# Kernel tuning notes

Hardware: AMD Instinct MI355X
Metric: run time of the kernel (lower is better)

## Reference

```python
import jax, jax.numpy as jnp
import numpy as np

B, S, E, H = 1, 2048, 512, 8
D = E // H
N = B * S
WIN_HALF = 32  # attention_window 64 -> +/-32
ALPHA = 0.1
LN_EPS = 1e-12
NEG_INF = -1e9


def _build_window_edges():
    # windowed graph: dst i attends to src j with |i-j| <= WIN_HALF, within each batch block
    i = np.arange(S)
    offs = np.arange(-WIN_HALF, WIN_HALF + 1)
    src = i[:, None] + offs[None, :]
    dst = np.broadcast_to(i[:, None], src.shape)
    valid = (src >= 0) & (src < S)
    src, dst = src[valid], dst[valid]
    srcs, dsts = [], []
    for b in range(B):
        srcs.append(src + b * S)
        dsts.append(dst + b * S)
    return (np.concatenate(srcs).astype(np.int32),
            np.concatenate(dsts).astype(np.int32))


def setup_inputs() -> dict:
    key = jax.random.key(0)
    ks = jax.random.split(key, 12)
    sc = 1.0 / np.sqrt(E)
    src_np, dst_np = _build_window_edges()
    return {
        "hidden_states": jax.random.normal(ks[0], (B, S, E), dtype=jnp.float32),
        "attention_mask": jnp.zeros((B, S), dtype=jnp.float32),
        "edge_src": jnp.asarray(src_np),
        "edge_dst": jnp.asarray(dst_np),
        "Wq": jax.random.normal(ks[1], (E, E), dtype=jnp.float32) * sc,
        "bq": jnp.zeros((E,), dtype=jnp.float32),
        "Wk": jax.random.normal(ks[2], (E, E), dtype=jnp.float32) * sc,
        "bk": jnp.zeros((E,), dtype=jnp.float32),
        "Wv": jax.random.normal(ks[3], (E, E), dtype=jnp.float32) * sc,
        "bv": jnp.zeros((E,), dtype=jnp.float32),
        "Wo": jax.random.normal(ks[4], (E, E), dtype=jnp.float32) * sc,
        "bo": jnp.zeros((E,), dtype=jnp.float32),
        "ln_g": jnp.ones((E,), dtype=jnp.float32),
        "ln_b": jnp.zeros((E,), dtype=jnp.float32),
    }


def reference(hidden_states, attention_mask, edge_src, edge_dst,
              Wq, bq, Wk, bk, Wv, bv, Wo, bo, ln_g, ln_b):
    x = hidden_states  # (B,S,E); node ordering n = b*S + s (matches torch reshape)
    q = ((x @ Wq + bq) / jnp.sqrt(jnp.asarray(D, x.dtype))).reshape(N, H, D)
    k = (x @ Wk + bk).reshape(N, H, D)
    v = (x @ Wv + bv).reshape(N, H, D)

    mask = (attention_mask >= 0).reshape(N)  # bool per node

    # u_dot_v('k','q','score'): per-edge, per-head dot product
    score = jnp.einsum('ehd,ehd->eh', k[edge_src], q[edge_dst])  # (Eg,H)
    score = jnp.where(mask[edge_src][:, None], score, NEG_INF)

    # edge_softmax over incoming edges of each destination node
    smax = jax.ops.segment_max(score, edge_dst, num_segments=N)
    p = jnp.exp(score - smax[edge_dst])
    denom = jax.ops.segment_sum(p, edge_dst, num_segments=N)
    p = p / denom[edge_dst]  # (Eg,H)

    # 5 diffusion steps: h <- A h, blended with residual v (dropout off in eval)
    h = v
    for _ in range(5):
        m = h[edge_src] * p[:, :, None]                      # u_mul_e
        h = jax.ops.segment_sum(m, edge_dst, num_segments=N)  # sum('m','h')
        h = (1.0 - ALPHA) * h + ALPHA * v

    attn = h.reshape(B, S, E)

    # DiffuserSelfOutput: dense -> residual add -> LayerNorm
    y = attn @ Wo + bo + hidden_states
    mu = y.mean(-1, keepdims=True)
    var = ((y - mu) ** 2).mean(-1, keepdims=True)
    out = (y - mu) * jax.lax.rsqrt(var + LN_EPS) * ln_g + ln_b
    return out
```

## Files before the change

### kernel.cpp

```cpp
#include <hip/hip_runtime.h>
#include <math.h>

#define S_LEN 2048
#define E_DIM 512
#define NE (S_LEN * E_DIM)
#define H_NUM 8
#define WH 32
#define NOFF 65
#define PROW (H_NUM * NOFF)
#define PN (S_LEN * PROW)

typedef float f32x4 __attribute__((ext_vector_type(4)));
typedef short short8 __attribute__((ext_vector_type(8)));

__device__ __forceinline__ unsigned short f2bf(float f) {
    union { float f; unsigned u; } cv; cv.f = f;
    unsigned u = cv.u;
    u += 0x7fffu + ((u >> 16) & 1u);
    return (unsigned short)(u >> 16);
}
__device__ __forceinline__ unsigned pk2(float x, float y) {
    return (unsigned)f2bf(x) | ((unsigned)f2bf(y) << 16);
}

__device__ __forceinline__ void mfma_gemm_f32(
    const float* __restrict__ A, const float* __restrict__ W,
    const float* __restrict__ bias, float* __restrict__ C,
    float scale, int m0, int n0)
{
    __shared__ unsigned short As[64 * 40];
    __shared__ unsigned short Bs[64 * 40];
    const int tid = threadIdx.x;
    const int lane = tid & 63, wave = tid >> 6;
    const int quad = lane >> 4, l16 = lane & 15;
    const int wr = (wave >> 1) * 32, wc = (wave & 1) * 32;
    const int ar = tid >> 2, ac = (tid & 3) * 8;
    const int bn = tid & 63, bk0 = (tid >> 6) * 8;

    f32x4 acc00 = {0.f,0.f,0.f,0.f}, acc01 = acc00, acc10 = acc00, acc11 = acc00;

    for (int kk = 0; kk < E_DIM; kk += 32) {
        float4 a0 = *(const float4*)(A + (size_t)(m0 + ar) * E_DIM + kk + ac);
        float4 a1 = *(const float4*)(A + (size_t)(m0 + ar) * E_DIM + kk + ac + 4);
        float b[8];
#pragma unroll
        for (int j = 0; j < 8; ++j)
            b[j] = W[(size_t)(kk + bk0 + j) * E_DIM + n0 + bn];
        __syncthreads();
        uint4 ap; ap.x = pk2(a0.x, a0.y); ap.y = pk2(a0.z, a0.w);
        ap.z = pk2(a1.x, a1.y); ap.w = pk2(a1.z, a1.w);
        *(uint4*)(As + ar * 40 + ac) = ap;
        uint4 bp; bp.x = pk2(b[0], b[1]); bp.y = pk2(b[2], b[3]);
        bp.z = pk2(b[4], b[5]); bp.w = pk2(b[6], b[7]);
        *(uint4*)(Bs + bn * 40 + bk0) = bp;
        __syncthreads();
        short8 fa0 = *(const short8*)(As + (wr + l16) * 40 + quad * 8);
        short8 fa1 = *(const short8*)(As + (wr + 16 + l16) * 40 + quad * 8);
        short8 fb0 = *(const short8*)(Bs + (wc + l16) * 40 + quad * 8);
        short8 fb1 = *(const short8*)(Bs + (wc + 16 + l16) * 40 + quad * 8);
        acc00 = __builtin_amdgcn_mfma_f32_16x16x32_bf16(fa0, fb0, acc00, 0, 0, 0);
        acc01 = __builtin_amdgcn_mfma_f32_16x16x32_bf16(fa0, fb1, acc01, 0, 0, 0);
        acc10 = __builtin_amdgcn_mfma_f32_16x16x32_bf16(fa1, fb0, acc10, 0, 0, 0);
        acc11 = __builtin_amdgcn_mfma_f32_16x16x32_bf16(fa1, fb1, acc11, 0, 0, 0);
    }

#pragma unroll
    for (int mi = 0; mi < 2; ++mi) {
#pragma unroll
        for (int ni = 0; ni < 2; ++ni) {
            f32x4 a = (mi == 0) ? ((ni == 0) ? acc00 : acc01)
                                : ((ni == 0) ? acc10 : acc11);
            int n = n0 + wc + ni * 16 + l16;
            float bval = bias[n];
#pragma unroll
            for (int r = 0; r < 4; ++r) {
                int m = m0 + wr + mi * 16 + quad * 4 + r;
                C[(size_t)m * E_DIM + n] = (a[r] + bval) * scale;
            }
        }
    }
}

__global__ __launch_bounds__(256)
void qkv_gemm(const float* __restrict__ x,
              const float* __restrict__ Wq, const float* __restrict__ bq,
              const float* __restrict__ Wk, const float* __restrict__ bk,
              const float* __restrict__ Wv, const float* __restrict__ bv,
              float* __restrict__ q, float* __restrict__ k, float* __restrict__ v)
{
    const float* W; const float* b; float* o; float sc;
    if (blockIdx.z == 0)      { W = Wq; b = bq; o = q; sc = 0.125f; }
    else if (blockIdx.z == 1) { W = Wk; b = bk; o = k; sc = 1.0f; }
    else                      { W = Wv; b = bv; o = v; sc = 1.0f; }
    mfma_gemm_f32(x, W, b, o, sc, blockIdx.y * 64, blockIdx.x * 64);
}

#define SDN 32
__global__ __launch_bounds__(256)
void scores_d1(const float* __restrict__ q, const float* __restrict__ k,
               const float* __restrict__ v, const float* __restrict__ amask,
               float* __restrict__ P, float* __restrict__ hA)
{
    const int i0 = blockIdx.x * SDN;
    const int h  = blockIdx.y;
    const int tid = threadIdx.x;
    __shared__ float ks[96 * 68];
    __shared__ float am[96];
    __shared__ float sc[SDN * 66];
    __shared__ float smx[SDN], sidn[SDN];
    __shared__ float ps[SDN * NOFF];

    for (int e = tid; e < 96 * 16; e += 256) {
        int lr = e >> 4, c4 = e & 15;
        int j = i0 - WH + lr;
        int jc = min(max(j, 0), S_LEN - 1);
        *(float4*)(ks + lr * 68 + c4 * 4) =
            *(const float4*)(k + (size_t)jc * E_DIM + h * 64 + c4 * 4);
    }
    if (tid < 96) {
        int j = i0 - WH + tid;
        am[tid] = (j >= 0 && j < S_LEN) ? amask[j] : -1.0f;
    }

    const int dst = tid >> 3;
    const int og  = tid & 7;
    float4 qreg[16];
    {
        const float4* qrow = (const float4*)(q + (size_t)(i0 + dst) * E_DIM + h * 64);
#pragma unroll
        for (int t = 0; t < 16; ++t) qreg[t] = qrow[t];
    }
    __syncthreads();

    for (int off = og; off < NOFF; off += 8) {
        int j = i0 + dst + off - WH;
        float s;
        if (j < 0 || j >= S_LEN) {
            s = -INFINITY;
        } else {
            int lr = dst + off;
            const float4* kr = (const float4*)(ks + lr * 68);
            float acc = 0.f;
#pragma unroll
            for (int t = 0; t < 16; ++t) {
                float4 a = qreg[t], bb = kr[t];
                acc += a.x * bb.x + a.y * bb.y + a.z * bb.z + a.w * bb.w;
            }
            s = (am[lr] >= 0.f) ? acc : -1e9f;
        }
        sc[dst * 66 + off] = s;
    }
    __syncthreads();

    for (int e = tid; e < 96 * 16; e += 256) {
        int lr = e >> 4, c4 = e & 15;
        int j = i0 - WH + lr;
        int jc = min(max(j, 0), S_LEN - 1);
        *(float4*)(ks + lr * 68 + c4 * 4) =
            *(const float4*)(v + (size_t)jc * E_DIM + h * 64 + c4 * 4);
    }
    if (tid < SDN) {
        float mx = -INFINITY;
        for (int o = 0; o < NOFF; ++o) mx = fmaxf(mx, sc[tid * 66 + o]);
        float dn = 0.f;
        for (int o = 0; o < NOFF; ++o) dn += expf(sc[tid * 66 + o] - mx);
        smx[tid] = mx; sidn[tid] = 1.f / dn;
    }
    __syncthreads();

    for (int e = tid; e < SDN * NOFF; e += 256) {
        int d = e / NOFF, off = e - d * NOFF;
        float pv = expf(sc[d * 66 + off] - smx[d]) * sidn[d];
        P[(size_t)(i0 + d) * PROW + h * NOFF + off] = pv;
        ps[e] = pv;
    }
    __syncthreads();

    {
        const int ci = tid & 15;
        const int ob = (tid >> 4) * 2;
        float4 a0 = {0,0,0,0}, a1 = a0;
        for (int lr = ob; lr < ob + 66; ++lr) {
            float4 hval = *(const float4*)(ks + lr * 68 + ci * 4);
            int o0 = lr - ob;
            if (o0 <= 64) {
                float p = ps[ob * NOFF + o0];
                a0.x += p * hval.x; a0.y += p * hval.y; a0.z += p * hval.z; a0.w += p * hval.w;
            }
            int o1 = o0 - 1;
            if ((unsigned)o1 <= 64u) {
                float p = ps[(ob + 1) * NOFF + o1];
                a1.x += p * hval.x; a1.y += p * hval.y; a1.z += p * hval.z; a1.w += p * hval.w;
            }
        }
#pragma unroll
        for (int r = 0; r < 2; ++r) {
            float4 a = r ? a1 : a0;
            float4 vv = *(const float4*)(ks + (WH + ob + r) * 68 + ci * 4);
            float4 o;
            o.x = 0.9f * a.x + 0.1f * vv.x;
            o.y = 0.9f * a.y + 0.1f * vv.y;
            o.z = 0.9f * a.z + 0.1f * vv.z;
            o.w = 0.9f * a.w + 0.1f * vv.w;
            *(float4*)(hA + (size_t)(i0 + ob + r) * E_DIM + h * 64 + ci * 4) = o;
        }
    }
}

__global__ __launch_bounds__(512)
void diffuse2c(const float* __restrict__ hin, const float* __restrict__ v,
               const float* __restrict__ P, float* __restrict__ hout)
{
    const int i0 = blockIdx.x * 64;
    const int c0 = blockIdx.y * 32;
    const int h  = c0 >> 6;
    const int tid = threadIdx.x;
    __shared__ float hs[192 * 36];
    __shared__ float h1[128 * 36];
    __shared__ float ps[128 * NOFF];

    for (int e = tid; e < 192 * 8; e += 512) {
        int lr = e >> 3, c4 = e & 7;
        int j = i0 - 64 + lr;
        int jc = min(max(j, 0), S_LEN - 1);
        *(float4*)(hs + lr * 36 + c4 * 4) =
            *(const float4*)(hin + (size_t)jc * E_DIM + c0 + c4 * 4);
    }
    for (int e = tid; e < 128 * NOFF; e += 512) {
        int mr = e / NOFF, o = e - mr * NOFF;
        int j = i0 - 32 + mr;
        int jc = min(max(j, 0), S_LEN - 1);
        ps[e] = P[(size_t)jc * PROW + h * NOFF + o];
    }
    __syncthreads();

    const int ci = tid & 7;
    const int g  = tid >> 3;

    {
        float4 a0 = {0,0,0,0}, a1 = a0;
        const int mb = g * 2;
        for (int lr = 0; lr < 66; ++lr) {
            float4 hval = *(const float4*)(hs + (mb + lr) * 36 + ci * 4);
            if (lr <= 64) {
                float p = ps[mb * NOFF + lr];
                a0.x += p * hval.x; a0.y += p * hval.y; a0.z += p * hval.z; a0.w += p * hval.w;
            }
            int o1 = lr - 1;
            if ((unsigned)o1 <= 64u) {
                float p = ps[(mb + 1) * NOFF + o1];
                a1.x += p * hval.x; a1.y += p * hval.y; a1.z += p * hval.z; a1.w += p * hval.w;
            }
        }
#pragma unroll
        for (int r = 0; r < 2; ++r) {
            float4 a = r ? a1 : a0;
            int j = i0 - 32 + mb + r;
            int jc = min(max(j, 0), S_LEN - 1);
            float4 vv = *(const float4*)(v + (size_t)jc * E_DIM + c0 + ci * 4);
            float4 o;
            o.x = 0.9f * a.x + 0.1f * vv.x;
            o.y = 0.9f * a.y + 0.1f * vv.y;
            o.z = 0.9f * a.z + 0.1f * vv.z;
            o.w = 0.9f * a.w + 0.1f * vv.w;
            *(float4*)(h1 + (mb + r) * 36 + ci * 4) = o;
        }
    }
    __syncthreads();

    {
        float4 a = {0,0,0,0};
        for (int off = 0; off < NOFF; ++off) {
            float4 hval = *(const float4*)(h1 + (g + off) * 36 + ci * 4);
            float p = ps[(g + 32) * NOFF + off];
            a.x += p * hval.x; a.y += p * hval.y; a.z += p * hval.z; a.w += p * hval.w;
        }
        size_t base = (size_t)(i0 + g) * E_DIM + c0 + ci * 4;
        float4 vv = *(const float4*)(v + base);
        float4 o;
        o.x = 0.9f * a.x + 0.1f * vv.x;
        o.y = 0.9f * a.y + 0.1f * vv.y;
        o.z = 0.9f * a.z + 0.1f * vv.z;
        o.w = 0.9f * a.w + 0.1f * vv.w;
        *(float4*)(hout + base) = o;
    }
}

__global__ __launch_bounds__(512)
void oln(const float* __restrict__ hsrc, const float* __restrict__ Wo,
         const float* __restrict__ bo, const float* __restrict__ x,
         const float* __restrict__ g, const float* __restrict__ lb,
         float* __restrict__ out)
{
    __shared__ unsigned short As[16 * 40];
    __shared__ unsigned short Bs[512 * 40];
    __shared__ float rsum[8][16], rsq[8][16];
    const int tid = threadIdx.x;
    const int lane = tid & 63, wave = tid >> 6;
    const int quad = lane >> 4, l16 = lane & 15;
    const int m0 = blockIdx.x * 16;
    const int n = tid;

    f32x4 acc[4];
#pragma unroll
    for (int t = 0; t < 4; ++t) acc[t] = (f32x4){0.f,0.f,0.f,0.f};

    for (int kk = 0; kk < E_DIM; kk += 32) {
        float4 av;
        if (tid < 128)
            av = *(const float4*)(hsrc + (size_t)(m0 + (tid >> 3)) * E_DIM + kk + (tid & 7) * 4);
        float bcol[32];
#pragma unroll
        for (int j = 0; j < 32; ++j)
            bcol[j] = Wo[(size_t)(kk + j) * E_DIM + n];
        __syncthreads();
        if (tid < 128) {
            uint2 ap; ap.x = pk2(av.x, av.y); ap.y = pk2(av.z, av.w);
            *(uint2*)(As + (tid >> 3) * 40 + (tid & 7) * 4) = ap;
        }
#pragma unroll
        for (int t = 0; t < 4; ++t) {
            uint4 bp;
            bp.x = pk2(bcol[t*8+0], bcol[t*8+1]); bp.y = pk2(bcol[t*8+2], bcol[t*8+3]);
            bp.z = pk2(bcol[t*8+4], bcol[t*8+5]); bp.w = pk2(bcol[t*8+6], bcol[t*8+7]);
            *(uint4*)(Bs + n * 40 + t * 8) = bp;
        }
        __syncthreads();
        short8 fa = *(const short8*)(As + l16 * 40 + quad * 8);
#pragma unroll
        for (int nt = 0; nt < 4; ++nt) {
            short8 fb = *(const short8*)(Bs + (wave * 64 + nt * 16 + l16) * 40 + quad * 8);
            acc[nt] = __builtin_amdgcn_mfma_f32_16x16x32_bf16(fa, fb, acc[nt], 0, 0, 0);
        }
    }

    float s[4] = {0.f,0.f,0.f,0.f}, s2[4] = {0.f,0.f,0.f,0.f};
#pragma unroll
    for (int nt = 0; nt < 4; ++nt) {
        int nc = wave * 64 + nt * 16 + l16;
        float bv = bo[nc];
#pragma unroll
        for (int r = 0; r < 4; ++r) {
            int m = m0 + quad * 4 + r;
            float vl = acc[nt][r] + bv + x[(size_t)m * E_DIM + nc];
            acc[nt][r] = vl;
            s[r] += vl; s2[r] += vl * vl;
        }
    }
#pragma unroll
    for (int o = 1; o < 16; o <<= 1) {
#pragma unroll
        for (int r = 0; r < 4; ++r) {
            s[r]  += __shfl_xor(s[r], o, 64);
            s2[r] += __shfl_xor(s2[r], o, 64);
        }
    }
    if (l16 == 0) {
#pragma unroll
        for (int r = 0; r < 4; ++r) {
            rsum[wave][quad * 4 + r] = s[r];
            rsq[wave][quad * 4 + r]  = s2[r];
        }
    }
    __syncthreads();
    float mu[4], rs[4];
#pragma unroll
    for (int r = 0; r < 4; ++r) {
        int rl = quad * 4 + r;
        float tot = 0.f, tot2 = 0.f;
#pragma unroll
        for (int w = 0; w < 8; ++w) { tot += rsum[w][rl]; tot2 += rsq[w][rl]; }
        float m_ = tot * (1.f / 512.f);
        float var = tot2 * (1.f / 512.f) - m_ * m_;
        mu[r] = m_; rs[r] = rsqrtf(var + 1e-12f);
    }
#pragma unroll
    for (int nt = 0; nt < 4; ++nt) {
        int nc = wave * 64 + nt * 16 + l16;
        float gv = g[nc], bbv = lb[nc];
#pragma unroll
        for (int r = 0; r < 4; ++r) {
            int m = m0 + quad * 4 + r;
            out[(size_t)m * E_DIM + nc] = (acc[nt][r] - mu[r]) * rs[r] * gv + bbv;
        }
    }
}

extern "C" void kernel_launch(void* const* d_in, const int* in_sizes, int n_in,
                              void* d_out, int out_size, void* d_ws, size_t ws_size,
                              hipStream_t stream)
{
    const float* x     = (const float*)d_in[0];
    const float* amask = (const float*)d_in[1];
    const float* Wq = (const float*)d_in[4];
    const float* bq = (const float*)d_in[5];
    const float* Wk = (const float*)d_in[6];
    const float* bk = (const float*)d_in[7];
    const float* Wv = (const float*)d_in[8];
    const float* bv = (const float*)d_in[9];
    const float* Wo = (const float*)d_in[10];
    const float* bo = (const float*)d_in[11];
    const float* lng = (const float*)d_in[12];
    const float* lnb = (const float*)d_in[13];
    float* out = (float*)d_out;

    float* ws = (float*)d_ws;
    float* q  = ws;
    float* k  = ws + (size_t)NE;
    float* v  = ws + (size_t)2 * NE;
    float* P  = ws + (size_t)3 * NE;
    float* hA = ws + (size_t)3 * NE + PN;
    float* hB = hA + (size_t)NE;

    qkv_gemm<<<dim3(8, 32, 3), 256, 0, stream>>>(x, Wq, bq, Wk, bk, Wv, bv, q, k, v);

    scores_d1<<<dim3(64, 8), 256, 0, stream>>>(q, k, v, amask, P, hA);

    diffuse2c<<<dim3(32, 16), 512, 0, stream>>>(hA, v, P, hB);
    diffuse2c<<<dim3(32, 16), 512, 0, stream>>>(hB, v, P, hA);

    oln<<<128, 512, 0, stream>>>(hA, Wo, bo, x, lng, lnb, out);
}
```

Before: 174.9 us.

## Rewrite two-step diffusion kernel as banded bf16 MFMA matmuls

Replaces the scalar FP32 two-step windowed diffusion kernel with one that treats each step as a banded matrix product. The probabilities and hidden states are converted to bf16 in transposed LDS layouts and multiplied with 16x16x32 bf16 MFMA instructions. Each block now covers a full head of 64 columns with 256 threads instead of 32 columns with 512 threads. The aim is to move the dominant FMA work onto matrix cores, at the cost of bf16 rounding of intermediate diffusion states and some wasted MACs on the zeroed band edges.

```diff
diff --git a/kernel.cpp b/kernel.cpp
--- a/kernel.cpp
+++ b/kernel.cpp
@@ -207,82 +207,129 @@
     }
 }
 
-__global__ __launch_bounds__(512)
-void diffuse2c(const float* __restrict__ hin, const float* __restrict__ v,
+__global__ __launch_bounds__(256)
+void diffuse2m(const float* __restrict__ hin, const float* __restrict__ v,
                const float* __restrict__ P, float* __restrict__ hout)
 {
+    __shared__ unsigned short hT[64 * 200];
+    __shared__ unsigned short m1T[64 * 136];
+    __shared__ unsigned short ps[128 * 68];
     const int i0 = blockIdx.x * 64;
-    const int c0 = blockIdx.y * 32;
-    const int h  = c0 >> 6;
-    const int tid = threadIdx.x;
-    __shared__ float hs[192 * 36];
-    __shared__ float h1[128 * 36];
-    __shared__ float ps[128 * NOFF];
-
-    for (int e = tid; e < 192 * 8; e += 512) {
-        int lr = e >> 3, c4 = e & 7;
-        int j = i0 - 64 + lr;
-        int jc = min(max(j, 0), S_LEN - 1);
-        *(float4*)(hs + lr * 36 + c4 * 4) =
-            *(const float4*)(hin + (size_t)jc * E_DIM + c0 + c4 * 4);
-    }
-    for (int e = tid; e < 128 * NOFF; e += 512) {
-        int mr = e / NOFF, o = e - mr * NOFF;
-        int j = i0 - 32 + mr;
-        int jc = min(max(j, 0), S_LEN - 1);
-        ps[e] = P[(size_t)jc * PROW + h * NOFF + o];
-    }
-    __syncthreads();
-
-    const int ci = tid & 7;
-    const int g  = tid >> 3;
-
-    {
-        float4 a0 = {0,0,0,0}, a1 = a0;
-        const int mb = g * 2;
-        for (int lr = 0; lr < 66; ++lr) {
-            float4 hval = *(const float4*)(hs + (mb + lr) * 36 + ci * 4);
-            if (lr <= 64) {
-                float p = ps[mb * NOFF + lr];
-                a0.x += p * hval.x; a0.y += p * hval.y; a0.z += p * hval.z; a0.w += p * hval.w;
-            }
-            int o1 = lr - 1;
-            if ((unsigned)o1 <= 64u) {
-                float p = ps[(mb + 1) * NOFF + o1];
-                a1.x += p * hval.x; a1.y += p * hval.y; a1.z += p * hval.z; a1.w += p * hval.w;
-            }
-        }
-#pragma unroll
-        for (int r = 0; r < 2; ++r) {
-            float4 a = r ? a1 : a0;
-            int j = i0 - 32 + mb + r;
-            int jc = min(max(j, 0), S_LEN - 1);
-            float4 vv = *(const float4*)(v + (size_t)jc * E_DIM + c0 + ci * 4);
-            float4 o;
-            o.x = 0.9f * a.x + 0.1f * vv.x;
-            o.y = 0.9f * a.y + 0.1f * vv.y;
-            o.z = 0.9f * a.z + 0.1f * vv.z;
-            o.w = 0.9f * a.w + 0.1f * vv.w;
-            *(float4*)(h1 + (mb + r) * 36 + ci * 4) = o;
-        }
-    }
-    __syncthreads();
-
-    {
-        float4 a = {0,0,0,0};
-        for (int off = 0; off < NOFF; ++off) {
-            float4 hval = *(const float4*)(h1 + (g + off) * 36 + ci * 4);
-            float p = ps[(g + 32) * NOFF + off];
-            a.x += p * hval.x; a.y += p * hval.y; a.z += p * hval.z; a.w += p * hval.w;
-        }
-        size_t base = (size_t)(i0 + g) * E_DIM + c0 + ci * 4;
-        float4 vv = *(const float4*)(v + base);
-        float4 o;
-        o.x = 0.9f * a.x + 0.1f * vv.x;
-        o.y = 0.9f * a.y + 0.1f * vv.y;
-        o.z = 0.9f * a.z + 0.1f * vv.z;
-        o.w = 0.9f * a.w + 0.1f * vv.w;
-        *(float4*)(hout + base) = o;
+    const int h  = blockIdx.y;
+    const int c0 = h * 64;
+    const int tid  = threadIdx.x;
+    const int lane = tid & 63, wave = tid >> 6;
+    const int quad = lane >> 4, l16 = lane & 15;
+
+    for (int e = tid; e < 96 * 16; e += 256) {
+        int lr2 = (e >> 4) * 2, c4 = (e & 15) * 4;
+        int ja = min(max(i0 - 64 + lr2,     0), S_LEN - 1);
+        int jb = min(max(i0 - 64 + lr2 + 1, 0), S_LEN - 1);
+        float4 ha = *(const float4*)(hin + (size_t)ja * E_DIM + c0 + c4);
+        float4 hb = *(const float4*)(hin + (size_t)jb * E_DIM + c0 + c4);
+        *(unsigned*)(hT + (c4 + 0) * 200 + lr2) = pk2(ha.x, hb.x);
+        *(unsigned*)(hT + (c4 + 1) * 200 + lr2) = pk2(ha.y, hb.y);
+        *(unsigned*)(hT + (c4 + 2) * 200 + lr2) = pk2(ha.z, hb.z);
+        *(unsigned*)(hT + (c4 + 3) * 200 + lr2) = pk2(ha.w, hb.w);
+    }
+    for (int e = tid; e < 128 * 33; e += 256) {
+        int mr = e / 33, t = e - mr * 33;
+        int jc = min(max(i0 - 32 + mr, 0), S_LEN - 1);
+        const float* pr = P + (size_t)jc * PROW + h * NOFF;
+        if (t < 32) {
+            *(unsigned*)(ps + mr * 68 + t * 2) = pk2(pr[t * 2], pr[t * 2 + 1]);
+        } else {
+            ps[mr * 68 + 64] = f2bf(pr[64]);
+        }
+    }
+    __syncthreads();
+
+    const int mt0 = wave * 32;
+    f32x4 acc1[2][4];
+#pragma unroll
+    for (int a = 0; a < 2; ++a)
+#pragma unroll
+        for (int b = 0; b < 4; ++b) acc1[a][b] = (f32x4){0.f,0.f,0.f,0.f};
+
+    for (int ks = wave; ks <= wave + 2; ++ks) {
+        const int k0q = ks * 32 + quad * 8;
+        short8 fb[4];
+#pragma unroll
+        for (int nt = 0; nt < 4; ++nt)
+            fb[nt] = *(const short8*)(hT + (nt * 16 + l16) * 200 + k0q);
+#pragma unroll
+        for (int mt = 0; mt < 2; ++mt) {
+            const int m = mt0 + mt * 16 + l16;
+            const int start = k0q - m;
+            short8 fa;
+#pragma unroll
+            for (int j = 0; j < 8; ++j) {
+                int idx = start + j;
+                int idc = min(max(idx, 0), 64);
+                unsigned short pv = ps[m * 68 + idc];
+                fa[j] = ((unsigned)idx <= 64u) ? (short)pv : (short)0;
+            }
+#pragma unroll
+            for (int nt = 0; nt < 4; ++nt)
+                acc1[mt][nt] = __builtin_amdgcn_mfma_f32_16x16x32_bf16(fa, fb[nt], acc1[mt][nt], 0, 0, 0);
+        }
+    }
+
+#pragma unroll
+    for (int mt = 0; mt < 2; ++mt) {
+#pragma unroll
+        for (int nt = 0; nt < 4; ++nt) {
+            int n = nt * 16 + l16;
+            int mbase = mt0 + mt * 16 + quad * 4;
+            float o[4];
+#pragma unroll
+            for (int r = 0; r < 4; ++r) {
+                int mgc = min(max(i0 - 32 + mbase + r, 0), S_LEN - 1);
+                float vv = v[(size_t)mgc * E_DIM + c0 + n];
+                o[r] = 0.9f * acc1[mt][nt][r] + 0.1f * vv;
+            }
+            uint2 pkd; pkd.x = pk2(o[0], o[1]); pkd.y = pk2(o[2], o[3]);
+            *(uint2*)(m1T + n * 136 + mbase) = pkd;
+        }
+    }
+    __syncthreads();
+
+    const int mt2 = wave * 16;
+    f32x4 acc2[4];
+#pragma unroll
+    for (int b = 0; b < 4; ++b) acc2[b] = (f32x4){0.f,0.f,0.f,0.f};
+
+    const int kslo = mt2 >> 5, kshi = (mt2 + 79) >> 5;
+    for (int ks = kslo; ks <= kshi; ++ks) {
+        const int k0q = ks * 32 + quad * 8;
+        short8 fb[4];
+#pragma unroll
+        for (int nt = 0; nt < 4; ++nt)
+            fb[nt] = *(const short8*)(m1T + (nt * 16 + l16) * 136 + k0q);
+        const int m = mt2 + l16;
+        const int start = k0q - m;
+        short8 fa;
+#pragma unroll
+        for (int j = 0; j < 8; ++j) {
+            int idx = start + j;
+            int idc = min(max(idx, 0), 64);
+            unsigned short pv = ps[(m + 32) * 68 + idc];
+            fa[j] = ((unsigned)idx <= 64u) ? (short)pv : (short)0;
+        }
+#pragma unroll
+        for (int nt = 0; nt < 4; ++nt)
+            acc2[nt] = __builtin_amdgcn_mfma_f32_16x16x32_bf16(fa, fb[nt], acc2[nt], 0, 0, 0);
+    }
+
+#pragma unroll
+    for (int nt = 0; nt < 4; ++nt) {
+        int n = nt * 16 + l16;
+#pragma unroll
+        for (int r = 0; r < 4; ++r) {
+            int m = mt2 + quad * 4 + r;
+            size_t base = (size_t)(i0 + m) * E_DIM + c0 + n;
+            hout[base] = 0.9f * acc2[nt][r] + 0.1f * v[base];
+        }
     }
 }
 
@@ -416,8 +463,8 @@
 
     scores_d1<<<dim3(64, 8), 256, 0, stream>>>(q, k, v, amask, P, hA);
 
-    diffuse2c<<<dim3(32, 16), 512, 0, stream>>>(hA, v, P, hB);
-    diffuse2c<<<dim3(32, 16), 512, 0, stream>>>(hB, v, P, hA);
+    diffuse2m<<<dim3(32, 8), 256, 0, stream>>>(hA, v, P, hB);
+    diffuse2m<<<dim3(32, 8), 256, 0, stream>>>(hB, v, P, hA);
 
     oln<<<128, 512, 0, stream>>>(hA, Wo, bo, x, lng, lnb, out);
 }
```

Result: no change. 175.6 us (+0.4%).
